# Kernel optimization log

Measured on AMD Instinct MI355X. Metric: run time of the kernel, lower is better.

Reference implementation:

```python
import jax, jax.numpy as jnp
import numpy as np


def setup_inputs() -> dict:
    key = jax.random.key(0)
    ks = jax.random.split(key, 8)
    B, C, N = 4, 64, 32768
    d = C // 8
    inp = {
        "x": jax.random.normal(ks[0], (B, C, N), dtype=jnp.float32),
        "Wq": jax.random.normal(ks[1], (d, C), dtype=jnp.float32) * 0.1,
        "bq": jax.random.normal(ks[2], (d,), dtype=jnp.float32) * 0.1,
        "Wk": jax.random.normal(ks[3], (d, C), dtype=jnp.float32) * 0.1,
        "bk": jax.random.normal(ks[4], (d,), dtype=jnp.float32) * 0.1,
        "Wv": jax.random.normal(ks[5], (C, C), dtype=jnp.float32) * 0.1,
        "bv": jax.random.normal(ks[6], (C,), dtype=jnp.float32) * 0.1,
        # nn.Parameter(torch.zeros(1)) in the original; nonzero here so the
        # attention branch actually contributes to the output.
        "gamma": jax.random.normal(ks[7], (1,), dtype=jnp.float32) * 0.1,
        "window_size": 512,
        "stride": 256,
        "pooling_factor": 2,
    }
    return inp


def reference(x, Wq, bq, Wk, bk, Wv, bv, gamma, window_size, stride, pooling_factor):
    B, C, N = x.shape
    # conv1x1 projections are pointwise -> apply once on the full signal
    q = jnp.einsum("dc,bcn->bdn", Wq, x) + bq[None, :, None]  # [B, d, N]
    k = jnp.einsum("dc,bcn->bdn", Wk, x) + bk[None, :, None]  # [B, d, N]
    v = jnp.einsum("ec,bcn->ben", Wv, x) + bv[None, :, None]  # [B, C, N]

    starts = jnp.arange(0, N - window_size + 1, stride)              # [W]
    idx = starts[:, None] + jnp.arange(window_size)[None, :]         # [W, ws]

    qw = q[:, :, idx]  # [B, d, W, ws]
    kw = k[:, :, idx]
    vw = v[:, :, idx]  # [B, C, W, ws]
    xw = x[:, :, idx]

    energy = jnp.einsum("bdwi,bdwj->bwij", qw, kw)                   # [B, W, ws, ws]
    attn = jax.nn.softmax(energy, axis=-1)
    # torch: bmm(v, attn^T) -> out[c,i] = sum_j v[c,j] * attn[i,j]
    out_local = jnp.einsum("bcwj,bwij->bcwi", vw, attn)              # [B, C, W, ws]

    contrib = gamma[0] * out_local + xw
    out = jnp.zeros_like(x).at[:, :, idx].add(contrib)               # overlap-add
    counts = jnp.zeros((N,), x.dtype).at[idx].add(1.0)               # overlap count
    out = out / counts[None, None, :]

    P = pooling_factor
    Np = (N // P) * P
    out = out[:, :, :Np].reshape(B, C, N // P, P).max(axis=-1)       # MaxPool1d(P)
    return out
```

## Files before the change

### kernel.cpp

```cpp
#include <hip/hip_runtime.h>
#include <hip/hip_bf16.h>

#define BB 4
#define CC 64
#define DD 8
#define NN 32768
#define WW 512
#define STR 256
#define NWIN 127
#define LOG2E 1.4426950408889634f

typedef short bf16x8 __attribute__((ext_vector_type(8)));
typedef float f32x4 __attribute__((ext_vector_type(4)));
typedef float f32x16 __attribute__((ext_vector_type(16)));

__device__ __forceinline__ unsigned int pack_bf16(float lo, float hi) {
    __hip_bfloat162 h = __float22bfloat162_rn(make_float2(lo, hi));
    unsigned int r; __builtin_memcpy(&r, &h, 4);
    return r;
}
__device__ __forceinline__ unsigned short to_bf16(float f) {
    __hip_bfloat16 h = __float2bfloat16(f);
    unsigned short r; __builtin_memcpy(&r, &h, 2);
    return r;
}
__device__ __forceinline__ float bf2f(unsigned short s) {
    union { unsigned int u; float f; } v; v.u = ((unsigned int)s) << 16;
    return v.f;
}
__device__ __forceinline__ float fast_exp2(float x) {
#if __has_builtin(__builtin_amdgcn_exp2f)
    return __builtin_amdgcn_exp2f(x);
#else
    float r; asm("v_exp_f32 %0, %1" : "=v"(r) : "v"(x)); return r;
#endif
}
__device__ __forceinline__ void plswap(unsigned int &x, unsigned int &y) {
    asm("v_permlane32_swap_b32 %0, %1" : "+v"(x), "+v"(y));
}
__device__ __forceinline__ bf16x8 pack8(float a0, float a1, float a2, float a3,
                                        float a4, float a5, float a6, float a7) {
    union { bf16x8 v; unsigned int u[4]; } r;
    r.u[0] = pack_bf16(a0, a1); r.u[1] = pack_bf16(a2, a3);
    r.u[2] = pack_bf16(a4, a5); r.u[3] = pack_bf16(a6, a7);
    return r.v;
}
__device__ __forceinline__ bf16x8 words4(unsigned int w0, unsigned int w1,
                                         unsigned int w2, unsigned int w3) {
    union { bf16x8 v; unsigned int u[4]; } r;
    r.u[0] = w0; r.u[1] = w1; r.u[2] = w2; r.u[3] = w3;
    return r.v;
}

__global__ __launch_bounds__(256) void qkv_kernel(
    const float* __restrict__ x,
    const float* __restrict__ Wq, const float* __restrict__ bq,
    const float* __restrict__ Wk, const float* __restrict__ bk,
    const float* __restrict__ Wv, const float* __restrict__ bv,
    unsigned short* __restrict__ qout, unsigned short* __restrict__ kout,
    unsigned short* __restrict__ vout)
{
    const int t = threadIdx.x;
    const int lane = t & 63, wv = t >> 6;
    const int a = lane & 15, g = lane >> 4;

    bf16x8 wf[5][2];
    #pragma unroll
    for (int T = 0; T < 5; ++T) {
        const float* wrow;
        float scale = 1.f;
        if (T == 0) {
            if (a < 8) { wrow = Wq + a*CC; scale = LOG2E; }
            else       { wrow = Wk + (a-8)*CC; }
        } else {
            wrow = Wv + ((T-1)*16 + a)*CC;
        }
        #pragma unroll
        for (int h = 0; h < 2; ++h) {
            float4 w0 = *(const float4*)(wrow + h*32 + g*8);
            float4 w1 = *(const float4*)(wrow + h*32 + g*8 + 4);
            wf[T][h] = pack8(w0.x*scale, w0.y*scale, w0.z*scale, w0.w*scale,
                             w1.x*scale, w1.y*scale, w1.z*scale, w1.w*scale);
        }
    }
    f32x4 bias[5];
    {
        const int r = g*4;
        #pragma unroll
        for (int u = 0; u < 4; ++u) {
            int rr = r + u;
            bias[0][u] = (rr < 8) ? bq[rr]*LOG2E : bk[rr-8];
        }
        #pragma unroll
        for (int T = 1; T < 5; ++T)
            #pragma unroll
            for (int u = 0; u < 4; ++u)
                bias[T][u] = bv[(T-1)*16 + r + u];
    }

    const int wave_id = blockIdx.x*4 + wv;
    #pragma unroll 1
    for (int it = 0; it < 2; ++it) {
        const int chunk = wave_id + it*4096;
        const int b = chunk >> 11;
        const int n0 = (chunk & 2047) * 16;
        const int n = n0 + a;
        const float* xcol = x + (size_t)b*CC*NN + n;

        float xv0[8], xv1[8];
        #pragma unroll
        for (int u = 0; u < 8; ++u) xv0[u] = xcol[(size_t)(g*8 + u)*NN];
        #pragma unroll
        for (int u = 0; u < 8; ++u) xv1[u] = xcol[(size_t)(32 + g*8 + u)*NN];
        bf16x8 xb0 = pack8(xv0[0],xv0[1],xv0[2],xv0[3],xv0[4],xv0[5],xv0[6],xv0[7]);
        bf16x8 xb1 = pack8(xv1[0],xv1[1],xv1[2],xv1[3],xv1[4],xv1[5],xv1[6],xv1[7]);

        f32x4 acc[5];
        #pragma unroll
        for (int T = 0; T < 5; ++T) {
            acc[T] = __builtin_amdgcn_mfma_f32_16x16x32_bf16(wf[T][0], xb0, bias[T], 0, 0, 0);
            acc[T] = __builtin_amdgcn_mfma_f32_16x16x32_bf16(wf[T][1], xb1, acc[T], 0, 0, 0);
        }

        {
            unsigned int lo = pack_bf16(acc[0][0], acc[0][1]);
            unsigned int hi = pack_bf16(acc[0][2], acc[0][3]);
            unsigned short* base = ((g < 2) ? qout : kout) + ((size_t)b*NN + n)*8 + (g & 1)*4;
            *(int2*)base = make_int2((int)lo, (int)hi);
        }
        #pragma unroll
        for (int T = 1; T < 5; ++T) {
            #pragma unroll
            for (int u = 0; u < 4; ++u) {
                const int e = (T-1)*16 + g*4 + u;
                vout[((size_t)b*CC + e)*NN + n] = to_bf16(acc[T][u]);
            }
        }
    }
}

__global__ __launch_bounds__(256) void attn_kernel(
    const unsigned short* __restrict__ qg, const unsigned short* __restrict__ kg,
    const unsigned short* __restrict__ vg,
    unsigned short* __restrict__ accE, unsigned short* __restrict__ accO)
{
    __shared__ float sInv[4][2][32];
    const int t = threadIdx.x;
    const int lane = t & 63, wv = t >> 6;
    const int l31 = lane & 31, hi = lane >> 5;
    int bid = blockIdx.x;
    const int ih = bid & 1; bid >>= 1;
    const int w = bid % NWIN, b = bid / NWIN;
    const int nwin = STR * w;
    const int i0 = ih*256 + wv*64;

    const unsigned short* qbase = qg + ((size_t)b*NN + nwin + i0)*8;
    const unsigned short* kbase = kg + ((size_t)b*NN + nwin)*8;
    const unsigned short* vbase = vg + (size_t)b*CC*NN + nwin;

    const bf16x8 zf = {};
    bf16x8 qf[2];
    #pragma unroll
    for (int it = 0; it < 2; ++it) {
        bf16x8 raw = *(const bf16x8*)(qbase + (size_t)(it*32 + l31)*8);
        qf[it] = hi ? zf : raw;
    }
    bf16x8 kc;
    {
        bf16x8 raw = *(const bf16x8*)(kbase + (size_t)l31*8);
        kc = hi ? zf : raw;
    }

    f32x16 acc[2][2] = {};
    float rsum[2] = {0.f, 0.f};

    for (int jt = 0; jt < 16; ++jt) {
        const int j0 = jt*32;
        bf16x8 vf[2][2];
        #pragma unroll
        for (int ct = 0; ct < 2; ++ct)
            #pragma unroll
            for (int sl = 0; sl < 2; ++sl)
                vf[ct][sl] = *(const bf16x8*)(vbase + (size_t)(ct*32 + l31)*NN + j0 + sl*16 + hi*8);
        bf16x8 kn = kc;
        if (jt < 15) {
            bf16x8 raw = *(const bf16x8*)(kbase + (size_t)(j0 + 32 + l31)*8);
            kn = hi ? zf : raw;
        }

        #pragma unroll
        for (int it = 0; it < 2; ++it) {
            const f32x16 z16 = {};
            f32x16 E = __builtin_amdgcn_mfma_f32_32x32x16_bf16(kc, qf[it], z16, 0, 0, 0);
            float p[16];
            #pragma unroll
            for (int r = 0; r < 16; ++r) p[r] = fast_exp2(E[r]);
            float s01 = (p[0]+p[1]) + (p[2]+p[3]);
            float s23 = (p[4]+p[5]) + (p[6]+p[7]);
            float s45 = (p[8]+p[9]) + (p[10]+p[11]);
            float s67 = (p[12]+p[13]) + (p[14]+p[15]);
            rsum[it] += (s01+s23) + (s45+s67);
            unsigned int wd[8];
            #pragma unroll
            for (int tw = 0; tw < 8; ++tw) wd[tw] = pack_bf16(p[2*tw], p[2*tw+1]);
            unsigned int F0 = wd[0], F2 = wd[2]; plswap(F0, F2);
            unsigned int F1 = wd[1], F3 = wd[3]; plswap(F1, F3);
            unsigned int G0 = wd[4], G2 = wd[6]; plswap(G0, G2);
            unsigned int G1 = wd[5], G3 = wd[7]; plswap(G1, G3);
            bf16x8 pa0 = words4(F0, F1, F2, F3);
            bf16x8 pa1 = words4(G0, G1, G2, G3);
            #pragma unroll
            for (int ct = 0; ct < 2; ++ct) {
                acc[it][ct] = __builtin_amdgcn_mfma_f32_32x32x16_bf16(pa0, vf[ct][0], acc[it][ct], 0, 0, 0);
                acc[it][ct] = __builtin_amdgcn_mfma_f32_32x32x16_bf16(pa1, vf[ct][1], acc[it][ct], 0, 0, 0);
            }
        }
        kc = kn;
    }

    #pragma unroll
    for (int it = 0; it < 2; ++it) rsum[it] += __shfl_xor(rsum[it], 32);
    if (lane < 32) {
        sInv[wv][0][lane] = 1.f / rsum[0];
        sInv[wv][1][lane] = 1.f / rsum[1];
    }
    f32x4 invv[2][4];
    #pragma unroll
    for (int it = 0; it < 2; ++it)
        #pragma unroll
        for (int g = 0; g < 4; ++g)
            invv[it][g] = *(const f32x4*)&sInv[wv][it][8*g + 4*hi];

    unsigned short* ob = ((w & 1) ? accO : accE) + (size_t)b*CC*NN + nwin + i0;
    #pragma unroll
    for (int it = 0; it < 2; ++it) {
        #pragma unroll
        for (int ct = 0; ct < 2; ++ct) {
            unsigned short* cbase = ob + (size_t)(ct*32 + l31)*NN + it*32;
            #pragma unroll
            for (int g = 0; g < 4; ++g) {
                float a0 = acc[it][ct][4*g+0] * invv[it][g][0];
                float a1 = acc[it][ct][4*g+1] * invv[it][g][1];
                float a2 = acc[it][ct][4*g+2] * invv[it][g][2];
                float a3 = acc[it][ct][4*g+3] * invv[it][g][3];
                int2 pw = make_int2((int)pack_bf16(a0, a1), (int)pack_bf16(a2, a3));
                *(int2*)(cbase + 8*g + 4*hi) = pw;
            }
        }
    }
}

__global__ __launch_bounds__(256) void final_kernel(
    const float* __restrict__ x,
    const unsigned short* __restrict__ accE, const unsigned short* __restrict__ accO,
    const float* __restrict__ gamma, float* __restrict__ out)
{
    const size_t tid = (size_t)blockIdx.x*256 + threadIdx.x;
    const size_t base = tid*8;
    const int n = (int)(base & (NN-1));
    const float g = gamma[0];

    float xv[8];
    *(float4*)&xv[0] = *(const float4*)&x[base];
    *(float4*)&xv[4] = *(const float4*)&x[base+4];
    int4 aeq = *(const int4*)&accE[base];
    const unsigned int* ae = (const unsigned int*)&aeq;

    float s[8];
    if (n >= STR && n < NN - STR) {
        int4 aoq = *(const int4*)&accO[base];
        const unsigned int* ao = (const unsigned int*)&aoq;
        #pragma unroll
        for (int u = 0; u < 4; ++u) {
            float e0 = bf2f((unsigned short)(ae[u] & 0xffff));
            float e1 = bf2f((unsigned short)(ae[u] >> 16));
            float o0 = bf2f((unsigned short)(ao[u] & 0xffff));
            float o1 = bf2f((unsigned short)(ao[u] >> 16));
            s[2*u]   = fmaf(g, (e0 + o0)*0.5f, xv[2*u]);
            s[2*u+1] = fmaf(g, (e1 + o1)*0.5f, xv[2*u+1]);
        }
    } else {
        #pragma unroll
        for (int u = 0; u < 4; ++u) {
            float e0 = bf2f((unsigned short)(ae[u] & 0xffff));
            float e1 = bf2f((unsigned short)(ae[u] >> 16));
            s[2*u]   = fmaf(g, e0, xv[2*u]);
            s[2*u+1] = fmaf(g, e1, xv[2*u+1]);
        }
    }
    float4 o = make_float4(fmaxf(s[0], s[1]), fmaxf(s[2], s[3]),
                           fmaxf(s[4], s[5]), fmaxf(s[6], s[7]));
    *(float4*)&out[tid*4] = o;
}

extern "C" void kernel_launch(void* const* d_in, const int* in_sizes, int n_in,
                              void* d_out, int out_size, void* d_ws, size_t ws_size,
                              hipStream_t stream)
{
    const float* x    = (const float*)d_in[0];
    const float* Wq   = (const float*)d_in[1];
    const float* bq   = (const float*)d_in[2];
    const float* Wk   = (const float*)d_in[3];
    const float* bk   = (const float*)d_in[4];
    const float* Wv   = (const float*)d_in[5];
    const float* bv   = (const float*)d_in[6];
    const float* gamma= (const float*)d_in[7];

    unsigned short* q    = (unsigned short*)d_ws;
    unsigned short* k    = q + (size_t)BB*NN*DD;
    unsigned short* v    = k + (size_t)BB*NN*DD;
    unsigned short* accE = v + (size_t)BB*CC*NN;
    unsigned short* accO = accE + (size_t)BB*CC*NN;
    float* out = (float*)d_out;

    qkv_kernel<<<1024, 256, 0, stream>>>(x, Wq, bq, Wk, bk, Wv, bv, q, k, v);
    attn_kernel<<<BB*NWIN*2, 256, 0, stream>>>(q, k, v, accE, accO);
    final_kernel<<<BB*CC*NN/8/256, 256, 0, stream>>>(x, accE, accO, gamma, out);
}
```

Baseline: 79.53 us.

## Split attention blocks across channel halves to raise occupancy

Each attention block now handles only 32 of the 64 value channels, doubling the grid and halving the accumulator registers, with launch bounds requesting 6 blocks per CU. This is meant to raise occupancy and latency hiding on the MFMA and exp path. In exchange, the QK^T energy, exp and row-sum work is recomputed once per channel half. The zero-masking of the upper-lane K fragment is also dropped, and a waitcnt is added before the LDS reads.

```diff
diff --git a/kernel.cpp b/kernel.cpp
--- a/kernel.cpp
+++ b/kernel.cpp
@@ -139,7 +139,7 @@
     }
 }
 
-__global__ __launch_bounds__(256) void attn_kernel(
+__global__ __launch_bounds__(256, 6) void attn_kernel(
     const unsigned short* __restrict__ qg, const unsigned short* __restrict__ kg,
     const unsigned short* __restrict__ vg,
     unsigned short* __restrict__ accE, unsigned short* __restrict__ accO)
@@ -149,6 +149,7 @@
     const int lane = t & 63, wv = t >> 6;
     const int l31 = lane & 31, hi = lane >> 5;
     int bid = blockIdx.x;
+    const int ch = bid & 1; bid >>= 1;
     const int ih = bid & 1; bid >>= 1;
     const int w = bid % NWIN, b = bid / NWIN;
     const int nwin = STR * w;
@@ -156,7 +157,7 @@
 
     const unsigned short* qbase = qg + ((size_t)b*NN + nwin + i0)*8;
     const unsigned short* kbase = kg + ((size_t)b*NN + nwin)*8;
-    const unsigned short* vbase = vg + (size_t)b*CC*NN + nwin;
+    const unsigned short* vbase = vg + ((size_t)b*CC + ch*32)*NN + nwin;
 
     const bf16x8 zf = {};
     bf16x8 qf[2];
@@ -165,28 +166,19 @@
         bf16x8 raw = *(const bf16x8*)(qbase + (size_t)(it*32 + l31)*8);
         qf[it] = hi ? zf : raw;
     }
-    bf16x8 kc;
-    {
-        bf16x8 raw = *(const bf16x8*)(kbase + (size_t)l31*8);
-        kc = hi ? zf : raw;
-    }
-
-    f32x16 acc[2][2] = {};
+    bf16x8 kc = *(const bf16x8*)(kbase + (size_t)l31*8);
+
+    f32x16 acc[2] = {};
     float rsum[2] = {0.f, 0.f};
 
     for (int jt = 0; jt < 16; ++jt) {
         const int j0 = jt*32;
-        bf16x8 vf[2][2];
-        #pragma unroll
-        for (int ct = 0; ct < 2; ++ct)
-            #pragma unroll
-            for (int sl = 0; sl < 2; ++sl)
-                vf[ct][sl] = *(const bf16x8*)(vbase + (size_t)(ct*32 + l31)*NN + j0 + sl*16 + hi*8);
+        bf16x8 vf[2];
+        #pragma unroll
+        for (int sl = 0; sl < 2; ++sl)
+            vf[sl] = *(const bf16x8*)(vbase + (size_t)l31*NN + j0 + sl*16 + hi*8);
         bf16x8 kn = kc;
-        if (jt < 15) {
-            bf16x8 raw = *(const bf16x8*)(kbase + (size_t)(j0 + 32 + l31)*8);
-            kn = hi ? zf : raw;
-        }
+        if (jt < 15) kn = *(const bf16x8*)(kbase + (size_t)(j0 + 32 + l31)*8);
 
         #pragma unroll
         for (int it = 0; it < 2; ++it) {
@@ -209,11 +201,8 @@
             unsigned int G1 = wd[5], G3 = wd[7]; plswap(G1, G3);
             bf16x8 pa0 = words4(F0, F1, F2, F3);
             bf16x8 pa1 = words4(G0, G1, G2, G3);
-            #pragma unroll
-            for (int ct = 0; ct < 2; ++ct) {
-                acc[it][ct] = __builtin_amdgcn_mfma_f32_32x32x16_bf16(pa0, vf[ct][0], acc[it][ct], 0, 0, 0);
-                acc[it][ct] = __builtin_amdgcn_mfma_f32_32x32x16_bf16(pa1, vf[ct][1], acc[it][ct], 0, 0, 0);
-            }
+            acc[it] = __builtin_amdgcn_mfma_f32_32x32x16_bf16(pa0, vf[0], acc[it], 0, 0, 0);
+            acc[it] = __builtin_amdgcn_mfma_f32_32x32x16_bf16(pa1, vf[1], acc[it], 0, 0, 0);
         }
         kc = kn;
     }
@@ -224,6 +213,7 @@
         sInv[wv][0][lane] = 1.f / rsum[0];
         sInv[wv][1][lane] = 1.f / rsum[1];
     }
+    __builtin_amdgcn_s_waitcnt(0);
     f32x4 invv[2][4];
     #pragma unroll
     for (int it = 0; it < 2; ++it)
@@ -231,21 +221,18 @@
         for (int g = 0; g < 4; ++g)
             invv[it][g] = *(const f32x4*)&sInv[wv][it][8*g + 4*hi];
 
-    unsigned short* ob = ((w & 1) ? accO : accE) + (size_t)b*CC*NN + nwin + i0;
+    unsigned short* ob = ((w & 1) ? accO : accE) + ((size_t)b*CC + ch*32)*NN + nwin + i0;
     #pragma unroll
     for (int it = 0; it < 2; ++it) {
-        #pragma unroll
-        for (int ct = 0; ct < 2; ++ct) {
-            unsigned short* cbase = ob + (size_t)(ct*32 + l31)*NN + it*32;
-            #pragma unroll
-            for (int g = 0; g < 4; ++g) {
-                float a0 = acc[it][ct][4*g+0] * invv[it][g][0];
-                float a1 = acc[it][ct][4*g+1] * invv[it][g][1];
-                float a2 = acc[it][ct][4*g+2] * invv[it][g][2];
-                float a3 = acc[it][ct][4*g+3] * invv[it][g][3];
-                int2 pw = make_int2((int)pack_bf16(a0, a1), (int)pack_bf16(a2, a3));
-                *(int2*)(cbase + 8*g + 4*hi) = pw;
-            }
+        unsigned short* cbase = ob + (size_t)l31*NN + it*32;
+        #pragma unroll
+        for (int g = 0; g < 4; ++g) {
+            float a0 = acc[it][4*g+0] * invv[it][g][0];
+            float a1 = acc[it][4*g+1] * invv[it][g][1];
+            float a2 = acc[it][4*g+2] * invv[it][g][2];
+            float a3 = acc[it][4*g+3] * invv[it][g][3];
+            int2 pw = make_int2((int)pack_bf16(a0, a1), (int)pack_bf16(a2, a3));
+            *(int2*)(cbase + 8*g + 4*hi) = pw;
         }
     }
 }
@@ -314,6 +301,6 @@
     float* out = (float*)d_out;
 
     qkv_kernel<<<1024, 256, 0, stream>>>(x, Wq, bq, Wk, bk, Wv, bv, q, k, v);
-    attn_kernel<<<BB*NWIN*2, 256, 0, stream>>>(q, k, v, accE, accO);
+    attn_kernel<<<BB*NWIN*4, 256, 0, stream>>>(q, k, v, accE, accO);
     final_kernel<<<BB*CC*NN/8/256, 256, 0, stream>>>(x, accE, accO, gamma, out);
 }
```

Result: slower. 300.0 us (+277.2%).
